# Kernel tuning notes

Hardware: AMD Instinct MI355X
Metric: run time of the kernel (lower is better)

The kernel has to match this reference:

```python
import jax, jax.numpy as jnp
import numpy as np

N_NODES = 100000
N_EDGES = 800000
NUM_FEATURES = 64
HIDDEN = 16
N_GRAPHS = 64


def setup_inputs() -> dict:
    key = jax.random.key(0)
    ks = jax.random.split(key, 12)
    x = jax.random.normal(ks[0], (N_NODES, NUM_FEATURES), dtype=jnp.float32)
    edge_index = jax.random.randint(ks[1], (2, N_EDGES), 0, N_NODES, dtype=jnp.int64)
    batch = jnp.sort(jax.random.randint(ks[2], (N_NODES,), 0, N_GRAPHS, dtype=jnp.int64))
    def glorot(k, shape):
        fan_in, fan_out = shape
        s = jnp.sqrt(2.0 / (fan_in + fan_out))
        return jax.random.normal(k, shape, dtype=jnp.float32) * s
    return {
        "x": x,
        "edge_index": edge_index,
        "batch": batch,
        "W1_rel": glorot(ks[3], (NUM_FEATURES, HIDDEN)),
        "W1_root": glorot(ks[4], (NUM_FEATURES, HIDDEN)),
        "b1": jnp.zeros((HIDDEN,), dtype=jnp.float32),
        "W2_rel": glorot(ks[5], (HIDDEN, HIDDEN)),
        "W2_root": glorot(ks[6], (HIDDEN, HIDDEN)),
        "b2": jnp.zeros((HIDDEN,), dtype=jnp.float32),
        "Wlin": glorot(ks[7], (HIDDEN, 1)),
        "blin": jnp.zeros((1,), dtype=jnp.float32),
    }


def _graph_conv(h, src, dst, W_rel, W_root, b):
    # PyG GraphConv: out_i = W_rel @ sum_{j->i} h_j + b + W_root @ h_i
    agg = jax.ops.segment_sum(h[src], dst, num_segments=h.shape[0])
    return agg @ W_rel + b + h @ W_root


def reference(x, edge_index, batch, W1_rel, W1_root, b1, W2_rel, W2_root, b2, Wlin, blin):
    src, dst = edge_index[0], edge_index[1]
    h = jax.nn.relu(_graph_conv(x, src, dst, W1_rel, W1_root, b1))
    # F.dropout(training=False) is identity at inference
    h = _graph_conv(h, src, dst, W2_rel, W2_root, b2)
    # global mean pool over graphs
    sums = jax.ops.segment_sum(h, batch, num_segments=N_GRAPHS)  # [G, H]
    counts = jax.ops.segment_sum(jnp.ones((h.shape[0],), dtype=h.dtype), batch, num_segments=N_GRAPHS)
    pooled = sums / jnp.maximum(counts, 1.0)[:, None]
    out = pooled @ Wlin + blin  # [G, 1]
    return out.squeeze(1)
```

## Files before the change

kernel.cpp:

```cpp
#include <hip/hip_runtime.h>
#include <hip/hip_fp16.h>

#define BUCKET_BITS 7
#define BUCKET_N    128
#define SEG_CAP     1280
#define EPB         4096
#define EPT         16
#define OVF_CAP     16384
#define MAXBUCK     1024

__global__ __launch_bounds__(256) void k_init(
    int* __restrict__ cursor, int* __restrict__ ovf_n,
    float* __restrict__ T1, float* __restrict__ T2,
    float* __restrict__ cntg, int nbuck, int n_graphs)
{
    const int i0 = blockIdx.x * 256 + threadIdx.x;
    for (int i = i0; i < nbuck; i += gridDim.x * 256) cursor[i * 16] = i * SEG_CAP;
    if (blockIdx.x == 0) {
        const int t = threadIdx.x;
        if (t < n_graphs) { T1[t] = 0.f; T2[t] = 0.f; cntg[t] = 0.f; }
        if (t == 0) *ovf_n = 0;
    }
}

__global__ __launch_bounds__(256) void k_scatter_bin(
    const int* __restrict__ src, const int* __restrict__ dst,
    int* __restrict__ cursor, int2* __restrict__ seg,
    int* __restrict__ ovf_n, int2* __restrict__ ovf,
    int n_edges, int nbuck)
{
    __shared__ int hist[MAXBUCK];
    __shared__ int base[MAXBUCK];
    const int t = threadIdx.x;
    for (int i = t; i < nbuck; i += 256) hist[i] = 0;
    __syncthreads();

    const int e0 = blockIdx.x * EPB;
    int es[EPT], ed[EPT], ep[EPT];
#pragma unroll
    for (int k = 0; k < EPT; ++k) {
        const int e = e0 + k * 256 + t;
        if (e < n_edges) {
            ed[k] = dst[e];
            es[k] = src[e];
            ep[k] = atomicAdd(&hist[ed[k] >> BUCKET_BITS], 1);
        } else ed[k] = -1;
    }
    __syncthreads();
    for (int b = t; b < nbuck; b += 256) {
        const int h = hist[b];
        base[b] = h ? atomicAdd(&cursor[b * 16], h) : 0;
    }
    __syncthreads();
#pragma unroll
    for (int k = 0; k < EPT; ++k) {
        if (ed[k] >= 0) {
            const int b = ed[k] >> BUCKET_BITS;
            const int addr = base[b] + ep[k];
            if (addr < (b + 1) * SEG_CAP) {
                seg[addr] = make_int2(es[k], ed[k]);
            } else {
                const int op = atomicAdd(ovf_n, 1);
                if (op < OVF_CAP) ovf[op] = make_int2(es[k], ed[k]);
            }
        }
    }
}

__global__ __launch_bounds__(256, 4) void k_transform1(
    const float* __restrict__ x, const float* __restrict__ Wrel,
    const float* __restrict__ Wroot, const float* __restrict__ bias,
    __half* __restrict__ p1, float* __restrict__ r1, int n_nodes)
{
    __shared__ float s_wr[1024];
    __shared__ float s_wo[1024];
    __shared__ float s_b[16];

    const int t = threadIdx.x;
    for (int i = t; i < 1024; i += 256) { s_wr[i] = Wrel[i]; s_wo[i] = Wroot[i]; }
    if (t < 16) s_b[t] = bias[t];
    __syncthreads();

    const int node = blockIdx.x * 256 + t;
    if (node >= n_nodes) return;

    float accr[16], acco[16];
#pragma unroll
    for (int o = 0; o < 16; ++o) { accr[o] = 0.f; acco[o] = 0.f; }

    const float* xr = x + (size_t)node * 64;
    for (int c = 0; c < 4; ++c) {
        float4 xv[4];
#pragma unroll
        for (int u = 0; u < 4; ++u) xv[u] = *(const float4*)(xr + c * 16 + u * 4);
#pragma unroll
        for (int u = 0; u < 4; ++u) {
            const float xs[4] = {xv[u].x, xv[u].y, xv[u].z, xv[u].w};
#pragma unroll
            for (int kk = 0; kk < 4; ++kk) {
                const int k = c * 16 + u * 4 + kk;
                const float xk = xs[kk];
                const float4* wr4 = (const float4*)&s_wr[k * 16];
                const float4* wo4 = (const float4*)&s_wo[k * 16];
#pragma unroll
                for (int q = 0; q < 4; ++q) {
                    const float4 wr = wr4[q], wo = wo4[q];
                    accr[q * 4 + 0] = fmaf(xk, wr.x, accr[q * 4 + 0]);
                    accr[q * 4 + 1] = fmaf(xk, wr.y, accr[q * 4 + 1]);
                    accr[q * 4 + 2] = fmaf(xk, wr.z, accr[q * 4 + 2]);
                    accr[q * 4 + 3] = fmaf(xk, wr.w, accr[q * 4 + 3]);
                    acco[q * 4 + 0] = fmaf(xk, wo.x, acco[q * 4 + 0]);
                    acco[q * 4 + 1] = fmaf(xk, wo.y, acco[q * 4 + 1]);
                    acco[q * 4 + 2] = fmaf(xk, wo.z, acco[q * 4 + 2]);
                    acco[q * 4 + 3] = fmaf(xk, wo.w, acco[q * 4 + 3]);
                }
            }
        }
    }

    __half2 ph[8];
#pragma unroll
    for (int k = 0; k < 8; ++k)
        ph[k] = __floats2half2_rn(accr[2 * k], accr[2 * k + 1]);
    ((uint4*)(p1 + (size_t)node * 16))[0] = ((const uint4*)ph)[0];
    ((uint4*)(p1 + (size_t)node * 16))[1] = ((const uint4*)ph)[1];
    float* rr = r1 + (size_t)node * 16;
#pragma unroll
    for (int q = 0; q < 4; ++q) {
        float4 v;
        v.x = acco[q * 4 + 0] + s_b[q * 4 + 0];
        v.y = acco[q * 4 + 1] + s_b[q * 4 + 1];
        v.z = acco[q * 4 + 2] + s_b[q * 4 + 2];
        v.w = acco[q * 4 + 3] + s_b[q * 4 + 3];
        *(float4*)(rr + q * 4) = v;
    }
}

__device__ inline void acc_half8(float* acc, uint4 raw) {
    const __half2* h2 = (const __half2*)&raw;
#pragma unroll
    for (int k = 0; k < 4; ++k) {
        const float2 f = __half22float2(h2[k]);
        acc[2 * k]     += f.x;
        acc[2 * k + 1] += f.y;
    }
}

__global__ __launch_bounds__(256) void k_aggregate(
    const __half* __restrict__ p1, const float* __restrict__ r1,
    const int2* __restrict__ seg, const int* __restrict__ cursor,
    const int* __restrict__ ovf_n, const int2* __restrict__ ovf,
    const int* __restrict__ batch,
    const float* __restrict__ W2rel, const float* __restrict__ W2root,
    const float* __restrict__ Wlin,
    float* __restrict__ s_out, float* __restrict__ T2, float* __restrict__ cntg,
    int* __restrict__ g_sorted, int* __restrict__ g_beg, int* __restrict__ g_cnt,
    int n_nodes)
{
    __shared__ int s_src[SEG_CAP];
    __shared__ int hist[BUCKET_N];
    __shared__ int iscan[BUCKET_N];
    __shared__ int cur[BUCKET_N];
    __shared__ float s_w2r[16], s_w2o[16];
    __shared__ float sT2[64], scnt[64];
    __shared__ int s_no, s_w0;

    const int t = threadIdx.x, b = blockIdx.x;
    if (t < BUCKET_N) hist[t] = 0;
    if (t < 16) {
        float ar = 0.f, ao = 0.f;
#pragma unroll
        for (int o = 0; o < 16; ++o) {
            const float wl = Wlin[o];
            ar = fmaf(W2rel[t * 16 + o], wl, ar);
            ao = fmaf(W2root[t * 16 + o], wl, ao);
        }
        s_w2r[t] = ar; s_w2o[t] = ao;
    }
    if (t < 64) { sT2[t] = 0.f; scnt[t] = 0.f; }
    if (t == 0) s_no = min(*ovf_n, OVF_CAP);
    __syncthreads();

    const int bstart = b * SEG_CAP;
    const int count = min(cursor[b * 16] - bstart, SEG_CAP);

    int2 er[5];
    int ne = 0;
    for (int i = t; i < count; i += 256) {
        er[ne] = seg[bstart + i];
        atomicAdd(&hist[er[ne].y & (BUCKET_N - 1)], 1);
        ++ne;
    }
    __syncthreads();
    int v = 0;
    if (t < BUCKET_N) {
        v = hist[t];
#pragma unroll
        for (int off = 1; off < 64; off <<= 1) {
            const int u = __shfl_up(v, off);
            if ((t & 63) >= off) v += u;
        }
        if (t == 63) s_w0 = v;
    }
    __syncthreads();
    if (t < BUCKET_N) {
        if (t >= 64) v += s_w0;
        iscan[t] = v;
        cur[t] = v - hist[t];
    }
    __syncthreads();
    for (int k = 0; k < ne; ++k)
        s_src[atomicAdd(&cur[er[k].y & (BUCKET_N - 1)], 1)] = er[k].x;
    __syncthreads();

    for (int i = t; i < count; i += 256) g_sorted[bstart + i] = s_src[i];
    if (t < BUCKET_N) {
        const int nodew = b * BUCKET_N + t;
        if (nodew < n_nodes) {
            g_beg[nodew] = bstart + iscan[t] - hist[t];
            g_cnt[nodew] = hist[t];
        }
    }

    const int nl = t >> 1, half = t & 1;
    const int node = b * BUCKET_N + nl;
    if (node < n_nodes) {
        const int end = iscan[nl];
        const int beg = end - hist[nl];
        float acc[8] = {0.f, 0.f, 0.f, 0.f, 0.f, 0.f, 0.f, 0.f};
        int j = beg;
        for (; j + 2 <= end; j += 2) {
            const int s0 = s_src[j], s1 = s_src[j + 1];
            const uint4 a = *(const uint4*)(p1 + (size_t)s0 * 16 + half * 8);
            const uint4 c = *(const uint4*)(p1 + (size_t)s1 * 16 + half * 8);
            acc_half8(acc, a);
            acc_half8(acc, c);
        }
        if (j < end) {
            const uint4 a = *(const uint4*)(p1 + (size_t)s_src[j] * 16 + half * 8);
            acc_half8(acc, a);
        }
        for (int ov = 0; ov < s_no; ++ov) {
            const int2 e = ovf[ov];
            if (e.y == node) {
                const uint4 a = *(const uint4*)(p1 + (size_t)e.x * 16 + half * 8);
                acc_half8(acc, a);
            }
        }
        const float4 rA = *(const float4*)(r1 + (size_t)node * 16 + half * 8);
        const float4 rB = *(const float4*)(r1 + (size_t)node * 16 + half * 8 + 4);
        float h[8];
        h[0] = fmaxf(acc[0] + rA.x, 0.f); h[1] = fmaxf(acc[1] + rA.y, 0.f);
        h[2] = fmaxf(acc[2] + rA.z, 0.f); h[3] = fmaxf(acc[3] + rA.w, 0.f);
        h[4] = fmaxf(acc[4] + rB.x, 0.f); h[5] = fmaxf(acc[5] + rB.y, 0.f);
        h[6] = fmaxf(acc[6] + rB.z, 0.f); h[7] = fmaxf(acc[7] + rB.w, 0.f);
        float ps = 0.f, pu = 0.f;
#pragma unroll
        for (int k = 0; k < 8; ++k) {
            ps = fmaf(h[k], s_w2r[half * 8 + k], ps);
            pu = fmaf(h[k], s_w2o[half * 8 + k], pu);
        }
        ps += __shfl_xor(ps, 1);
        pu += __shfl_xor(pu, 1);
        if (half == 0) {
            s_out[node] = ps;
            const int g = batch[node];
            atomicAdd(&sT2[g], pu);
            atomicAdd(&scnt[g], 1.f);
        }
    }
    __syncthreads();
    if (t < 64) {
        if (sT2[t] != 0.f) unsafeAtomicAdd(&T2[t], sT2[t]);
        if (scnt[t] != 0.f) unsafeAtomicAdd(&cntg[t], scnt[t]);
    }
}

__global__ __launch_bounds__(256) void k_T1(
    const float* __restrict__ s_in, const int* __restrict__ g_sorted,
    const int* __restrict__ g_beg, const int* __restrict__ g_cnt,
    const int* __restrict__ batch,
    const int* __restrict__ ovf_n, const int2* __restrict__ ovf,
    float* __restrict__ T1, int n_nodes)
{
    __shared__ float bins[64];
    const int t = threadIdx.x;
    if (t < 64) bins[t] = 0.f;
    __syncthreads();

    const int node = blockIdx.x * 256 + t;
    if (node < n_nodes) {
        const int beg = g_beg[node], c = g_cnt[node];
        float acc = 0.f;
        int j = 0;
        for (; j + 4 <= c; j += 4) {
            const int a = g_sorted[beg + j],      b2 = g_sorted[beg + j + 1];
            const int cc = g_sorted[beg + j + 2], d = g_sorted[beg + j + 3];
            acc += s_in[a] + s_in[b2] + s_in[cc] + s_in[d];
        }
        for (; j < c; ++j) acc += s_in[g_sorted[beg + j]];
        if (acc != 0.f) atomicAdd(&bins[batch[node]], acc);
    }
    __syncthreads();
    if (t < 64 && bins[t] != 0.f) unsafeAtomicAdd(&T1[t], bins[t]);

    if (blockIdx.x == 0) {
        const int n = min(*ovf_n, OVF_CAP);
        for (int i = t; i < n; i += 256)
            unsafeAtomicAdd(&T1[batch[ovf[i].y]], s_in[ovf[i].x]);
    }
}

__global__ void k_finalize(
    const float* __restrict__ T1, const float* __restrict__ T2,
    const float* __restrict__ cntg, const float* __restrict__ b2,
    const float* __restrict__ Wlin, const float* __restrict__ blin,
    float* __restrict__ out, int n_graphs)
{
    const int g = threadIdx.x;
    if (g >= n_graphs) return;
    float cb = 0.f;
#pragma unroll
    for (int o = 0; o < 16; ++o) cb = fmaf(b2[o], Wlin[o], cb);
    const float c = fmaxf(cntg[g], 1.f);
    out[g] = (T1[g] + T2[g]) / c + cb + blin[0];
}

extern "C" void kernel_launch(void* const* d_in, const int* in_sizes, int n_in,
                              void* d_out, int out_size, void* d_ws, size_t ws_size,
                              hipStream_t stream) {
    const float* x       = (const float*)d_in[0];
    const int*   ei      = (const int*)d_in[1];
    const int*   batch   = (const int*)d_in[2];
    const float* W1_rel  = (const float*)d_in[3];
    const float* W1_root = (const float*)d_in[4];
    const float* b1      = (const float*)d_in[5];
    const float* W2_rel  = (const float*)d_in[6];
    const float* W2_root = (const float*)d_in[7];
    const float* b2      = (const float*)d_in[8];
    const float* Wlin    = (const float*)d_in[9];
    const float* blin    = (const float*)d_in[10];
    float* out = (float*)d_out;

    const int N = in_sizes[0] / 64;
    const int E = in_sizes[1] / 2;
    const int G = out_size;
    const int nbuck = (N + BUCKET_N - 1) >> BUCKET_BITS;

    const int* src = ei;
    const int* dst = ei + E;

    auto rnd4 = [](size_t v) { return (v + 3) & ~(size_t)3; };
    float* ws = (float*)d_ws;
    size_t off = 0;
    __half* p1      = (__half*)(ws + off); off += rnd4((size_t)N * 8);
    float* r1       = ws + off; off += rnd4((size_t)N * 16);
    float* s_buf    = ws + off; off += rnd4((size_t)N);
    int*   cursor   = (int*)(ws + off); off += rnd4((size_t)nbuck * 16);
    int2*  seg      = (int2*)(ws + off); off += rnd4((size_t)nbuck * SEG_CAP * 2);
    int*   g_sorted = (int*)(ws + off); off += rnd4((size_t)nbuck * SEG_CAP);
    int*   g_beg    = (int*)(ws + off); off += rnd4((size_t)N);
    int*   g_cnt    = (int*)(ws + off); off += rnd4((size_t)N);
    int2*  ovf      = (int2*)(ws + off); off += rnd4((size_t)OVF_CAP * 2);
    int*   ovf_n    = (int*)(ws + off); off += 4;
    float* T1       = ws + off; off += rnd4((size_t)G);
    float* T2       = ws + off; off += rnd4((size_t)G);
    float* cntg     = ws + off; off += rnd4((size_t)G);

    const int sb = (E + EPB - 1) / EPB;
    const int tb = (N + 255) / 256;
    const int ab = (N + 255) / 256;

    k_init       <<<8, 256, 0, stream>>>(cursor, ovf_n, T1, T2, cntg, nbuck, G);
    k_scatter_bin<<<sb, 256, 0, stream>>>(src, dst, cursor, seg, ovf_n, ovf, E, nbuck);
    k_transform1 <<<tb, 256, 0, stream>>>(x, W1_rel, W1_root, b1, p1, r1, N);
    k_aggregate  <<<nbuck, 256, 0, stream>>>(p1, r1, seg, cursor, ovf_n, ovf, batch,
                                             W2_rel, W2_root, Wlin, s_buf, T2, cntg,
                                             g_sorted, g_beg, g_cnt, N);
    k_T1         <<<ab, 256, 0, stream>>>(s_buf, g_sorted, g_beg, g_cnt, batch,
                                          ovf_n, ovf, T1, N);
    k_finalize   <<<1, 64, 0, stream>>>(T1, T2, cntg, b2, Wlin, blin, out, G);
}
```

Measured before the change: 171.1 us.

## Merge transform and edge binning into one launch, replace init kernel with memset

The node transform kernel and the edge scatter/binning kernel are merged into one launch, with blocks partitioned by index, so the two independent stages run concurrently and one launch is saved. The init kernel is replaced by a single hipMemsetAsync over a contiguous workspace region, which required reordering the workspace layout and switching the cursor to relative offsets. This removes launch gaps and lets the compute-bound transform overlap with the atomic-heavy binning. The transform path also drops its launch_bounds occupancy hint of 4, which may change its register allocation.

Result: faster. 158.8 us (-7.2%).

```diff
diff --git a/kernel.cpp b/kernel.cpp
--- a/kernel.cpp
+++ b/kernel.cpp
@@ -9,130 +9,115 @@
 #define OVF_CAP     16384
 #define MAXBUCK     1024
 
-__global__ __launch_bounds__(256) void k_init(
-    int* __restrict__ cursor, int* __restrict__ ovf_n,
-    float* __restrict__ T1, float* __restrict__ T2,
-    float* __restrict__ cntg, int nbuck, int n_graphs)
-{
-    const int i0 = blockIdx.x * 256 + threadIdx.x;
-    for (int i = i0; i < nbuck; i += gridDim.x * 256) cursor[i * 16] = i * SEG_CAP;
-    if (blockIdx.x == 0) {
-        const int t = threadIdx.x;
-        if (t < n_graphs) { T1[t] = 0.f; T2[t] = 0.f; cntg[t] = 0.f; }
-        if (t == 0) *ovf_n = 0;
-    }
-}
-
-__global__ __launch_bounds__(256) void k_scatter_bin(
+__global__ __launch_bounds__(256) void k_phase1(
+    const float* __restrict__ x, const float* __restrict__ Wrel,
+    const float* __restrict__ Wroot, const float* __restrict__ bias,
     const int* __restrict__ src, const int* __restrict__ dst,
+    __half* __restrict__ p1, float* __restrict__ r1,
     int* __restrict__ cursor, int2* __restrict__ seg,
     int* __restrict__ ovf_n, int2* __restrict__ ovf,
-    int n_edges, int nbuck)
+    int n_nodes, int n_edges, int nbuck, int tb)
 {
-    __shared__ int hist[MAXBUCK];
-    __shared__ int base[MAXBUCK];
+    __shared__ int smem[2080];
     const int t = threadIdx.x;
-    for (int i = t; i < nbuck; i += 256) hist[i] = 0;
-    __syncthreads();
-
-    const int e0 = blockIdx.x * EPB;
-    int es[EPT], ed[EPT], ep[EPT];
-#pragma unroll
-    for (int k = 0; k < EPT; ++k) {
-        const int e = e0 + k * 256 + t;
-        if (e < n_edges) {
-            ed[k] = dst[e];
-            es[k] = src[e];
-            ep[k] = atomicAdd(&hist[ed[k] >> BUCKET_BITS], 1);
-        } else ed[k] = -1;
-    }
-    __syncthreads();
-    for (int b = t; b < nbuck; b += 256) {
-        const int h = hist[b];
-        base[b] = h ? atomicAdd(&cursor[b * 16], h) : 0;
-    }
-    __syncthreads();
-#pragma unroll
-    for (int k = 0; k < EPT; ++k) {
-        if (ed[k] >= 0) {
-            const int b = ed[k] >> BUCKET_BITS;
-            const int addr = base[b] + ep[k];
-            if (addr < (b + 1) * SEG_CAP) {
-                seg[addr] = make_int2(es[k], ed[k]);
-            } else {
-                const int op = atomicAdd(ovf_n, 1);
-                if (op < OVF_CAP) ovf[op] = make_int2(es[k], ed[k]);
-            }
-        }
-    }
-}
-
-__global__ __launch_bounds__(256, 4) void k_transform1(
-    const float* __restrict__ x, const float* __restrict__ Wrel,
-    const float* __restrict__ Wroot, const float* __restrict__ bias,
-    __half* __restrict__ p1, float* __restrict__ r1, int n_nodes)
-{
-    __shared__ float s_wr[1024];
-    __shared__ float s_wo[1024];
-    __shared__ float s_b[16];
-
-    const int t = threadIdx.x;
-    for (int i = t; i < 1024; i += 256) { s_wr[i] = Wrel[i]; s_wo[i] = Wroot[i]; }
-    if (t < 16) s_b[t] = bias[t];
-    __syncthreads();
-
-    const int node = blockIdx.x * 256 + t;
-    if (node >= n_nodes) return;
-
-    float accr[16], acco[16];
-#pragma unroll
-    for (int o = 0; o < 16; ++o) { accr[o] = 0.f; acco[o] = 0.f; }
-
-    const float* xr = x + (size_t)node * 64;
-    for (int c = 0; c < 4; ++c) {
-        float4 xv[4];
-#pragma unroll
-        for (int u = 0; u < 4; ++u) xv[u] = *(const float4*)(xr + c * 16 + u * 4);
-#pragma unroll
-        for (int u = 0; u < 4; ++u) {
-            const float xs[4] = {xv[u].x, xv[u].y, xv[u].z, xv[u].w};
-#pragma unroll
-            for (int kk = 0; kk < 4; ++kk) {
-                const int k = c * 16 + u * 4 + kk;
-                const float xk = xs[kk];
-                const float4* wr4 = (const float4*)&s_wr[k * 16];
-                const float4* wo4 = (const float4*)&s_wo[k * 16];
-#pragma unroll
-                for (int q = 0; q < 4; ++q) {
-                    const float4 wr = wr4[q], wo = wo4[q];
-                    accr[q * 4 + 0] = fmaf(xk, wr.x, accr[q * 4 + 0]);
-                    accr[q * 4 + 1] = fmaf(xk, wr.y, accr[q * 4 + 1]);
-                    accr[q * 4 + 2] = fmaf(xk, wr.z, accr[q * 4 + 2]);
-                    accr[q * 4 + 3] = fmaf(xk, wr.w, accr[q * 4 + 3]);
-                    acco[q * 4 + 0] = fmaf(xk, wo.x, acco[q * 4 + 0]);
-                    acco[q * 4 + 1] = fmaf(xk, wo.y, acco[q * 4 + 1]);
-                    acco[q * 4 + 2] = fmaf(xk, wo.z, acco[q * 4 + 2]);
-                    acco[q * 4 + 3] = fmaf(xk, wo.w, acco[q * 4 + 3]);
+
+    if ((int)blockIdx.x < tb) {
+        float* s_wr = (float*)smem;
+        float* s_wo = (float*)(smem + 1024);
+        float* s_b  = (float*)(smem + 2048);
+        for (int i = t; i < 1024; i += 256) { s_wr[i] = Wrel[i]; s_wo[i] = Wroot[i]; }
+        if (t < 16) s_b[t] = bias[t];
+        __syncthreads();
+
+        const int node = blockIdx.x * 256 + t;
+        if (node >= n_nodes) return;
+
+        float accr[16], acco[16];
+#pragma unroll
+        for (int o = 0; o < 16; ++o) { accr[o] = 0.f; acco[o] = 0.f; }
+
+        const float* xr = x + (size_t)node * 64;
+        for (int c = 0; c < 4; ++c) {
+            float4 xv[4];
+#pragma unroll
+            for (int u = 0; u < 4; ++u) xv[u] = *(const float4*)(xr + c * 16 + u * 4);
+#pragma unroll
+            for (int u = 0; u < 4; ++u) {
+                const float xs[4] = {xv[u].x, xv[u].y, xv[u].z, xv[u].w};
+#pragma unroll
+                for (int kk = 0; kk < 4; ++kk) {
+                    const int k = c * 16 + u * 4 + kk;
+                    const float xk = xs[kk];
+                    const float4* wr4 = (const float4*)&s_wr[k * 16];
+                    const float4* wo4 = (const float4*)&s_wo[k * 16];
+#pragma unroll
+                    for (int q = 0; q < 4; ++q) {
+                        const float4 wr = wr4[q], wo = wo4[q];
+                        accr[q * 4 + 0] = fmaf(xk, wr.x, accr[q * 4 + 0]);
+                        accr[q * 4 + 1] = fmaf(xk, wr.y, accr[q * 4 + 1]);
+                        accr[q * 4 + 2] = fmaf(xk, wr.z, accr[q * 4 + 2]);
+                        accr[q * 4 + 3] = fmaf(xk, wr.w, accr[q * 4 + 3]);
+                        acco[q * 4 + 0] = fmaf(xk, wo.x, acco[q * 4 + 0]);
+                        acco[q * 4 + 1] = fmaf(xk, wo.y, acco[q * 4 + 1]);
+                        acco[q * 4 + 2] = fmaf(xk, wo.z, acco[q * 4 + 2]);
+                        acco[q * 4 + 3] = fmaf(xk, wo.w, acco[q * 4 + 3]);
+                    }
                 }
             }
         }
-    }
-
-    __half2 ph[8];
-#pragma unroll
-    for (int k = 0; k < 8; ++k)
-        ph[k] = __floats2half2_rn(accr[2 * k], accr[2 * k + 1]);
-    ((uint4*)(p1 + (size_t)node * 16))[0] = ((const uint4*)ph)[0];
-    ((uint4*)(p1 + (size_t)node * 16))[1] = ((const uint4*)ph)[1];
-    float* rr = r1 + (size_t)node * 16;
-#pragma unroll
-    for (int q = 0; q < 4; ++q) {
-        float4 v;
-        v.x = acco[q * 4 + 0] + s_b[q * 4 + 0];
-        v.y = acco[q * 4 + 1] + s_b[q * 4 + 1];
-        v.z = acco[q * 4 + 2] + s_b[q * 4 + 2];
-        v.w = acco[q * 4 + 3] + s_b[q * 4 + 3];
-        *(float4*)(rr + q * 4) = v;
+
+        __half2 ph[8];
+#pragma unroll
+        for (int k = 0; k < 8; ++k)
+            ph[k] = __floats2half2_rn(accr[2 * k], accr[2 * k + 1]);
+        ((uint4*)(p1 + (size_t)node * 16))[0] = ((const uint4*)ph)[0];
+        ((uint4*)(p1 + (size_t)node * 16))[1] = ((const uint4*)ph)[1];
+        float* rr = r1 + (size_t)node * 16;
+#pragma unroll
+        for (int q = 0; q < 4; ++q) {
+            float4 v;
+            v.x = acco[q * 4 + 0] + s_b[q * 4 + 0];
+            v.y = acco[q * 4 + 1] + s_b[q * 4 + 1];
+            v.z = acco[q * 4 + 2] + s_b[q * 4 + 2];
+            v.w = acco[q * 4 + 3] + s_b[q * 4 + 3];
+            *(float4*)(rr + q * 4) = v;
+        }
+    } else {
+        int* hist = smem;
+        int* base = smem + 1024;
+        for (int i = t; i < nbuck; i += 256) hist[i] = 0;
+        __syncthreads();
+
+        const int e0 = ((int)blockIdx.x - tb) * EPB;
+        int es[EPT], ed[EPT], ep[EPT];
+#pragma unroll
+        for (int k = 0; k < EPT; ++k) {
+            const int e = e0 + k * 256 + t;
+            if (e < n_edges) {
+                ed[k] = dst[e];
+                es[k] = src[e];
+                ep[k] = atomicAdd(&hist[ed[k] >> BUCKET_BITS], 1);
+            } else ed[k] = -1;
+        }
+        __syncthreads();
+        for (int b = t; b < nbuck; b += 256) {
+            const int h = hist[b];
+            base[b] = h ? atomicAdd(&cursor[b * 16], h) : 0;
+        }
+        __syncthreads();
+#pragma unroll
+        for (int k = 0; k < EPT; ++k) {
+            if (ed[k] >= 0) {
+                const int b = ed[k] >> BUCKET_BITS;
+                const int rel = base[b] + ep[k];
+                if (rel < SEG_CAP) {
+                    seg[b * SEG_CAP + rel] = make_int2(es[k], ed[k]);
+                } else {
+                    const int op = atomicAdd(ovf_n, 1);
+                    if (op < OVF_CAP) ovf[op] = make_int2(es[k], ed[k]);
+                }
+            }
+        }
     }
 }
 
@@ -182,7 +167,7 @@
     __syncthreads();
 
     const int bstart = b * SEG_CAP;
-    const int count = min(cursor[b * 16] - bstart, SEG_CAP);
+    const int count = min(cursor[b * 16], SEG_CAP);
 
     int2 er[5];
     int ne = 0;
@@ -357,27 +342,29 @@
     float* r1       = ws + off; off += rnd4((size_t)N * 16);
     float* s_buf    = ws + off; off += rnd4((size_t)N);
     int*   cursor   = (int*)(ws + off); off += rnd4((size_t)nbuck * 16);
+    int*   ovf_n    = (int*)(ws + off); off += 4;
+    float* T1       = ws + off; off += rnd4((size_t)G);
+    float* T2       = ws + off; off += rnd4((size_t)G);
+    float* cntg     = ws + off; off += rnd4((size_t)G);
     int2*  seg      = (int2*)(ws + off); off += rnd4((size_t)nbuck * SEG_CAP * 2);
     int*   g_sorted = (int*)(ws + off); off += rnd4((size_t)nbuck * SEG_CAP);
     int*   g_beg    = (int*)(ws + off); off += rnd4((size_t)N);
     int*   g_cnt    = (int*)(ws + off); off += rnd4((size_t)N);
     int2*  ovf      = (int2*)(ws + off); off += rnd4((size_t)OVF_CAP * 2);
-    int*   ovf_n    = (int*)(ws + off); off += 4;
-    float* T1       = ws + off; off += rnd4((size_t)G);
-    float* T2       = ws + off; off += rnd4((size_t)G);
-    float* cntg     = ws + off; off += rnd4((size_t)G);
-
+
+    hipMemsetAsync(cursor, 0, ((size_t)nbuck * 16 + 4 + 3 * rnd4((size_t)G)) * sizeof(int), stream);
+
+    const int tb = (N + 255) / 256;
     const int sb = (E + EPB - 1) / EPB;
-    const int tb = (N + 255) / 256;
     const int ab = (N + 255) / 256;
 
-    k_init       <<<8, 256, 0, stream>>>(cursor, ovf_n, T1, T2, cntg, nbuck, G);
-    k_scatter_bin<<<sb, 256, 0, stream>>>(src, dst, cursor, seg, ovf_n, ovf, E, nbuck);
-    k_transform1 <<<tb, 256, 0, stream>>>(x, W1_rel, W1_root, b1, p1, r1, N);
-    k_aggregate  <<<nbuck, 256, 0, stream>>>(p1, r1, seg, cursor, ovf_n, ovf, batch,
-                                             W2_rel, W2_root, Wlin, s_buf, T2, cntg,
-                                             g_sorted, g_beg, g_cnt, N);
-    k_T1         <<<ab, 256, 0, stream>>>(s_buf, g_sorted, g_beg, g_cnt, batch,
-                                          ovf_n, ovf, T1, N);
-    k_finalize   <<<1, 64, 0, stream>>>(T1, T2, cntg, b2, Wlin, blin, out, G);
-}
+    k_phase1   <<<tb + sb, 256, 0, stream>>>(x, W1_rel, W1_root, b1, src, dst,
+                                             p1, r1, cursor, seg, ovf_n, ovf,
+                                             N, E, nbuck, tb);
+    k_aggregate<<<nbuck, 256, 0, stream>>>(p1, r1, seg, cursor, ovf_n, ovf, batch,
+                                           W2_rel, W2_root, Wlin, s_buf, T2, cntg,
+                                           g_sorted, g_beg, g_cnt, N);
+    k_T1       <<<ab, 256, 0, stream>>>(s_buf, g_sorted, g_beg, g_cnt, batch,
+                                        ovf_n, ovf, T1, N);
+    k_finalize <<<1, 64, 0, stream>>>(T1, T2, cntg, b2, Wlin, blin, out, G);
+}
```
